# Kernel optimization log

Hardware: AMD Instinct MI355X
Metric: run time of the kernel (lower is better)

Reference implementation:

```python
import jax, jax.numpy as jnp
import numpy as np

P = 1_500_000
N_DEPTH = 6 * 118 * 16 * 44  # 498432 flattened depth bins
N_FEAT = 6 * 16 * 44         # 4224 flattened feature rows
TOTAL_BEV = 40000            # 200x200 BEV grid
C = 80


def setup_inputs() -> dict:
    key = jax.random.key(0)
    k1, k2, k3, k4, k5, k6, k7 = jax.random.split(key, 7)
    depth = jax.random.uniform(k1, (6, 118, 16, 44), dtype=jnp.float32)
    feat = jax.random.normal(k2, (6, 16, 44, C), dtype=jnp.float32)
    ranks_depth = jax.random.randint(k3, (P,), 0, N_DEPTH, dtype=jnp.int64)
    ranks_feat = jax.random.randint(k4, (P,), 0, N_FEAT, dtype=jnp.int64)
    ranks_bev = jnp.sort(jax.random.randint(k5, (P,), 0, TOTAL_BEV, dtype=jnp.int64))
    interval_starts = jnp.sort(jax.random.randint(k6, (TOTAL_BEV,), 0, P, dtype=jnp.int64))
    interval_lengths = jax.random.randint(k7, (TOTAL_BEV,), 0, 64, dtype=jnp.int64)
    return {
        "depth": depth,
        "feat": feat,
        "ranks_depth": ranks_depth,
        "ranks_feat": ranks_feat,
        "ranks_bev": ranks_bev,
        "interval_starts": interval_starts,
        "interval_lengths": interval_lengths,
        "total_bev": TOTAL_BEV,
    }


def reference(depth, feat, ranks_depth, ranks_feat, ranks_bev,
              interval_starts, interval_lengths, total_bev):
    # interval_starts / interval_lengths are unused (as in the torch source)
    channels = feat.shape[-1]
    feat_flat = feat.reshape(-1, channels).astype(jnp.float32)   # [N_feat, C]
    depth_flat = depth.reshape(-1).astype(jnp.float32)           # [N_depth]
    gathered_feat = feat_flat[ranks_feat]                        # [P, C]
    gathered_depth = depth_flat[ranks_depth][:, None]            # [P, 1]
    weighted_feat = gathered_feat * gathered_depth               # [P, C]
    out = jax.ops.segment_sum(weighted_feat, ranks_bev,
                              num_segments=int(total_bev))       # [total_bev, C]
    return out
```

## Files before the change

kernel.cpp:

```cpp
#include <hip/hip_runtime.h>


#define CHN 80
#define SSTRIDE 84

__global__ __launch_bounds__(256)
void seg_starts_kernel(const int* __restrict__ rb, int* __restrict__ seg,
                       int P, int total_bev) {
    int q = blockIdx.x * blockDim.x + threadIdx.x;
    int i4 = q * 4;
    if (i4 >= P) return;
    const int4 v = *reinterpret_cast<const int4*>(rb + i4);
    int prev = (i4 == 0) ? -1 : rb[i4 - 1];
    int cur;
    cur = v.x; for (int b = prev + 1; b <= cur; ++b) seg[b] = i4 + 0; prev = cur;
    cur = v.y; for (int b = prev + 1; b <= cur; ++b) seg[b] = i4 + 1; prev = cur;
    cur = v.z; for (int b = prev + 1; b <= cur; ++b) seg[b] = i4 + 2; prev = cur;
    cur = v.w; for (int b = prev + 1; b <= cur; ++b) seg[b] = i4 + 3; prev = cur;
    if (i4 + 4 >= P) {
        for (int b = prev + 1; b <= total_bev; ++b) seg[b] = P;
    }
}

__global__ __launch_bounds__(256)
void bev_pool_kernel(const float* __restrict__ depth,
                     const float* __restrict__ feat,
                     const int* __restrict__ rd,
                     const int* __restrict__ rf,
                     const int* __restrict__ seg,
                     float* __restrict__ out,
                     int total_bev) {
    __shared__ float lds_buf[4][16 * SSTRIDE];

    const int wave = threadIdx.x >> 6;
    const int lane = threadIdx.x & 63;
    const int bin = blockIdx.x * 4 + wave;
    if (bin >= total_bev) return;

    const int slot = lane >> 2;
    const int ll   = lane & 3;

    const int lo = seg[bin];
    const int hi = seg[bin + 1];

    float4 a0 = make_float4(0.f, 0.f, 0.f, 0.f);
    float4 a1 = a0, a2 = a0, a3 = a0, a4 = a0;

    int i = lo + slot;
    bool valid = i < hi;
    int di = 0, fi = 0;
    if (valid) { di = rd[i]; fi = rf[i]; }
    while (valid) {
        const int ni = i + 16;
        const bool nvalid = ni < hi;
        int ndi = 0, nfi = 0;
        if (nvalid) { ndi = rd[ni]; nfi = rf[ni]; }

        const float d = depth[di];
        const float4* frow = reinterpret_cast<const float4*>(feat + (size_t)fi * CHN) + ll;
        const float4 f0 = frow[0];
        const float4 f1 = frow[4];
        const float4 f2 = frow[8];
        const float4 f3 = frow[12];
        const float4 f4 = frow[16];
        a0.x += d * f0.x; a0.y += d * f0.y; a0.z += d * f0.z; a0.w += d * f0.w;
        a1.x += d * f1.x; a1.y += d * f1.y; a1.z += d * f1.z; a1.w += d * f1.w;
        a2.x += d * f2.x; a2.y += d * f2.y; a2.z += d * f2.z; a2.w += d * f2.w;
        a3.x += d * f3.x; a3.y += d * f3.y; a3.z += d * f3.z; a3.w += d * f3.w;
        a4.x += d * f4.x; a4.y += d * f4.y; a4.z += d * f4.z; a4.w += d * f4.w;

        i = ni; di = ndi; fi = nfi; valid = nvalid;
    }

    {
        float* wb = &lds_buf[wave][slot * SSTRIDE + 4 * ll];
        *reinterpret_cast<float4*>(wb +  0) = a0;
        *reinterpret_cast<float4*>(wb + 16) = a1;
        *reinterpret_cast<float4*>(wb + 32) = a2;
        *reinterpret_cast<float4*>(wb + 48) = a3;
        *reinterpret_cast<float4*>(wb + 64) = a4;
    }
    const int g = lane >> 5;
    const int c = lane & 31;
    float4 r = make_float4(0.f, 0.f, 0.f, 0.f);
    if (c < 20) {
        const float* rp = &lds_buf[wave][g * 8 * SSTRIDE + c * 4];
        #pragma unroll
        for (int t = 0; t < 8; ++t) {
            const float4 v = *reinterpret_cast<const float4*>(rp + t * SSTRIDE);
            r.x += v.x; r.y += v.y; r.z += v.z; r.w += v.w;
        }
    }
    r.x += __shfl_xor(r.x, 32, 64);
    r.y += __shfl_xor(r.y, 32, 64);
    r.z += __shfl_xor(r.z, 32, 64);
    r.w += __shfl_xor(r.w, 32, 64);

    if (lane < 20) {
        *reinterpret_cast<float4*>(out + (size_t)bin * CHN + lane * 4) = r;
    }
}

extern "C" void kernel_launch(void* const* d_in, const int* in_sizes, int n_in,
                              void* d_out, int out_size, void* d_ws, size_t ws_size,
                              hipStream_t stream) {
    const float* depth = (const float*)d_in[0];
    const float* feat  = (const float*)d_in[1];
    const int*   rd    = (const int*)d_in[2];
    const int*   rf    = (const int*)d_in[3];
    const int*   rb    = (const int*)d_in[4];
    float* out = (float*)d_out;

    const int P = in_sizes[2];
    const int total_bev = out_size / CHN;

    int* seg = (int*)d_ws;

    const int quads = (P + 3) / 4;
    seg_starts_kernel<<<(quads + 255) / 256, 256, 0, stream>>>(rb, seg, P, total_bev);
    bev_pool_kernel<<<(total_bev + 3) / 4, 256, 0, stream>>>(depth, feat, rd, rf, seg,
                                                             out, total_bev);
}
```

Measured before the change: 114.6 us.

## Pack features to fp16 rows and pre-gather depth weights before pooling

Adds a pre-pass that converts the feature table to fp16 rows padded to 192 bytes, so the pooling loop reads half the bytes per gathered row. A second pre-pass gathers depth[ranks_depth] into a contiguous array, which turns the dependent random depth load into a streaming read inside the main loop. Which path runs depends on the available workspace size. The costs are two extra kernel launches, an extra P-sized write and read for the weights, and reduced feature precision that could affect accuracy tolerance.

Result: no change. 116.6 us (+1.7%).

```diff
diff --git a/kernel.cpp b/kernel.cpp
--- a/kernel.cpp
+++ b/kernel.cpp
@@ -1,8 +1,47 @@
 #include <hip/hip_runtime.h>
+#include <hip/hip_fp16.h>
 
 
 #define CHN 80
 #define SSTRIDE 84
+#define ROWB 192
+
+struct __align__(8)  h4 { __half2 a, b; };
+struct __align__(16) h8 { __half2 a, b, c, d; };
+
+__global__ __launch_bounds__(256)
+void gather_wd(const float* __restrict__ depth, const int* __restrict__ rd,
+               float* __restrict__ wd, int P) {
+    int q = blockIdx.x * blockDim.x + threadIdx.x;
+    int i4 = q * 4;
+    if (i4 + 3 < P) {
+        const int4 r = *reinterpret_cast<const int4*>(rd + i4);
+        float4 o;
+        o.x = depth[r.x]; o.y = depth[r.y]; o.z = depth[r.z]; o.w = depth[r.w];
+        *reinterpret_cast<float4*>(wd + i4) = o;
+    } else {
+        for (int i = i4; i < P; ++i) wd[i] = depth[rd[i]];
+    }
+}
+
+__global__ __launch_bounds__(256)
+void pack_feat_f16(const float* __restrict__ feat, __half* __restrict__ featp,
+                   int n_chunks ) {
+    int q = blockIdx.x * blockDim.x + threadIdx.x;
+    if (q >= n_chunks) return;
+    const int j = q / 24;
+    const int c = q - j * 24;
+    h4 o;
+    if (c < 20) {
+        const float4 v = *reinterpret_cast<const float4*>(feat + (size_t)j * CHN + c * 4);
+        o.a = __floats2half2_rn(v.x, v.y);
+        o.b = __floats2half2_rn(v.z, v.w);
+    } else {
+        o.a = __floats2half2_rn(0.f, 0.f);
+        o.b = o.a;
+    }
+    *reinterpret_cast<h4*>(reinterpret_cast<char*>(featp) + (size_t)j * ROWB + c * 8) = o;
+}
 
 __global__ __launch_bounds__(256)
 void seg_starts_kernel(const int* __restrict__ rb, int* __restrict__ seg,
@@ -22,9 +61,12 @@
     }
 }
 
+template <int MODE>
 __global__ __launch_bounds__(256)
 void bev_pool_kernel(const float* __restrict__ depth,
                      const float* __restrict__ feat,
+                     const __half* __restrict__ featp,
+                     const float* __restrict__ wd,
                      const int* __restrict__ rd,
                      const int* __restrict__ rf,
                      const int* __restrict__ seg,
@@ -49,36 +91,70 @@
     int i = lo + slot;
     bool valid = i < hi;
     int di = 0, fi = 0;
-    if (valid) { di = rd[i]; fi = rf[i]; }
+    float dv = 0.f;
+    if (valid) {
+        fi = rf[i];
+        if constexpr (MODE == 2) dv = wd[i]; else di = rd[i];
+    }
     while (valid) {
         const int ni = i + 16;
         const bool nvalid = ni < hi;
         int ndi = 0, nfi = 0;
-        if (nvalid) { ndi = rd[ni]; nfi = rf[ni]; }
-
-        const float d = depth[di];
-        const float4* frow = reinterpret_cast<const float4*>(feat + (size_t)fi * CHN) + ll;
-        const float4 f0 = frow[0];
-        const float4 f1 = frow[4];
-        const float4 f2 = frow[8];
-        const float4 f3 = frow[12];
-        const float4 f4 = frow[16];
-        a0.x += d * f0.x; a0.y += d * f0.y; a0.z += d * f0.z; a0.w += d * f0.w;
-        a1.x += d * f1.x; a1.y += d * f1.y; a1.z += d * f1.z; a1.w += d * f1.w;
-        a2.x += d * f2.x; a2.y += d * f2.y; a2.z += d * f2.z; a2.w += d * f2.w;
-        a3.x += d * f3.x; a3.y += d * f3.y; a3.z += d * f3.z; a3.w += d * f3.w;
-        a4.x += d * f4.x; a4.y += d * f4.y; a4.z += d * f4.z; a4.w += d * f4.w;
-
-        i = ni; di = ndi; fi = nfi; valid = nvalid;
+        float ndv = 0.f;
+        if (nvalid) {
+            nfi = rf[ni];
+            if constexpr (MODE == 2) ndv = wd[ni]; else ndi = rd[ni];
+        }
+
+        const float d = (MODE == 2) ? dv : depth[di];
+        if constexpr (MODE >= 1) {
+            const char* rowp = reinterpret_cast<const char*>(featp) + (size_t)fi * ROWB;
+            const h8 u0 = *reinterpret_cast<const h8*>(rowp + (ll << 4));
+            const h8 u1 = *reinterpret_cast<const h8*>(rowp + 64 + (ll << 4));
+            const h4 u2 = *reinterpret_cast<const h4*>(rowp + 128 + (ll << 3));
+            float2 p, q;
+            p = __half22float2(u0.a); q = __half22float2(u0.b);
+            a0.x += d*p.x; a0.y += d*p.y; a0.z += d*q.x; a0.w += d*q.y;
+            p = __half22float2(u0.c); q = __half22float2(u0.d);
+            a1.x += d*p.x; a1.y += d*p.y; a1.z += d*q.x; a1.w += d*q.y;
+            p = __half22float2(u1.a); q = __half22float2(u1.b);
+            a2.x += d*p.x; a2.y += d*p.y; a2.z += d*q.x; a2.w += d*q.y;
+            p = __half22float2(u1.c); q = __half22float2(u1.d);
+            a3.x += d*p.x; a3.y += d*p.y; a3.z += d*q.x; a3.w += d*q.y;
+            p = __half22float2(u2.a); q = __half22float2(u2.b);
+            a4.x += d*p.x; a4.y += d*p.y; a4.z += d*q.x; a4.w += d*q.y;
+        } else {
+            const float4* frow = reinterpret_cast<const float4*>(feat + (size_t)fi * CHN) + ll;
+            const float4 f0 = frow[0];
+            const float4 f1 = frow[4];
+            const float4 f2 = frow[8];
+            const float4 f3 = frow[12];
+            const float4 f4 = frow[16];
+            a0.x += d * f0.x; a0.y += d * f0.y; a0.z += d * f0.z; a0.w += d * f0.w;
+            a1.x += d * f1.x; a1.y += d * f1.y; a1.z += d * f1.z; a1.w += d * f1.w;
+            a2.x += d * f2.x; a2.y += d * f2.y; a2.z += d * f2.z; a2.w += d * f2.w;
+            a3.x += d * f3.x; a3.y += d * f3.y; a3.z += d * f3.z; a3.w += d * f3.w;
+            a4.x += d * f4.x; a4.y += d * f4.y; a4.z += d * f4.z; a4.w += d * f4.w;
+        }
+
+        i = ni; di = ndi; fi = nfi; dv = ndv; valid = nvalid;
     }
 
     {
-        float* wb = &lds_buf[wave][slot * SSTRIDE + 4 * ll];
-        *reinterpret_cast<float4*>(wb +  0) = a0;
-        *reinterpret_cast<float4*>(wb + 16) = a1;
-        *reinterpret_cast<float4*>(wb + 32) = a2;
-        *reinterpret_cast<float4*>(wb + 48) = a3;
-        *reinterpret_cast<float4*>(wb + 64) = a4;
+        float* wb = &lds_buf[wave][slot * SSTRIDE];
+        if constexpr (MODE >= 1) {
+            *reinterpret_cast<float4*>(wb + 8 * ll)      = a0;
+            *reinterpret_cast<float4*>(wb + 8 * ll + 4)  = a1;
+            *reinterpret_cast<float4*>(wb + 32 + 8 * ll) = a2;
+            *reinterpret_cast<float4*>(wb + 36 + 8 * ll) = a3;
+            *reinterpret_cast<float4*>(wb + 64 + 4 * ll) = a4;
+        } else {
+            *reinterpret_cast<float4*>(wb + 4 * ll)      = a0;
+            *reinterpret_cast<float4*>(wb + 4 * ll + 16) = a1;
+            *reinterpret_cast<float4*>(wb + 4 * ll + 32) = a2;
+            *reinterpret_cast<float4*>(wb + 4 * ll + 48) = a3;
+            *reinterpret_cast<float4*>(wb + 4 * ll + 64) = a4;
+        }
     }
     const int g = lane >> 5;
     const int c = lane & 31;
@@ -112,12 +188,37 @@
     float* out = (float*)d_out;
 
     const int P = in_sizes[2];
+    const int feat_elems = in_sizes[1];
+    const int n_rows = feat_elems / CHN;
     const int total_bev = out_size / CHN;
 
     int* seg = (int*)d_ws;
+    const size_t seg_bytes   = ((size_t)(total_bev + 1) * 4 + 255) & ~(size_t)255;
+    const size_t featp_bytes = (((size_t)n_rows * ROWB) + 255) & ~(size_t)255;
+    const size_t need_B = seg_bytes + featp_bytes;
+    const size_t need_A = need_B + (size_t)P * 4;
+    __half* featp = (__half*)((char*)d_ws + seg_bytes);
+    float*  wd    = (float*)((char*)d_ws + seg_bytes + featp_bytes);
+
+    const bool rows_ok = (feat_elems % CHN) == 0;
+    const int mode = (!rows_ok) ? 0 : (ws_size >= need_A) ? 2 : (ws_size >= need_B) ? 1 : 0;
 
     const int quads = (P + 3) / 4;
+    if (mode == 2) {
+        gather_wd<<<(quads + 255) / 256, 256, 0, stream>>>(depth, rd, wd, P);
+    }
+    if (mode >= 1) {
+        const int n_chunks = n_rows * 24;
+        pack_feat_f16<<<(n_chunks + 255) / 256, 256, 0, stream>>>(feat, featp, n_chunks);
+    }
     seg_starts_kernel<<<(quads + 255) / 256, 256, 0, stream>>>(rb, seg, P, total_bev);
-    bev_pool_kernel<<<(total_bev + 3) / 4, 256, 0, stream>>>(depth, feat, rd, rf, seg,
-                                                             out, total_bev);
-}
+
+    const int grid = (total_bev + 3) / 4;
+    if (mode == 2) {
+        bev_pool_kernel<2><<<grid, 256, 0, stream>>>(depth, feat, featp, wd, rd, rf, seg, out, total_bev);
+    } else if (mode == 1) {
+        bev_pool_kernel<1><<<grid, 256, 0, stream>>>(depth, feat, featp, wd, rd, rf, seg, out, total_bev);
+    } else {
+        bev_pool_kernel<0><<<grid, 256, 0, stream>>>(depth, feat, featp, wd, rd, rf, seg, out, total_bev);
+    }
+}
```

## Stage fp16 feature channel slices in LDS and pre-gather depth weights

Applied to the files above, without the earlier changes.

Adds a pre-pass that gathers depth[ranks_depth] into a contiguous workspace array. The main kernel splits the 80 channels into 10 groups of 8, and each block stages all feature rows for its group in LDS as fp16. Each block then processes a chunk of bins, reading features from LDS instead of doing random global float4 gathers. This costs an extra kernel launch and P*4 bytes of workspace, re-reads rf/wd ten times (once per channel group), and reduces feature precision to half.

Result: slower. 289.6 us (+152.7%).

```diff
diff --git a/kernel.cpp b/kernel.cpp
--- a/kernel.cpp
+++ b/kernel.cpp
@@ -1,8 +1,30 @@
 #include <hip/hip_runtime.h>
+#include <hip/hip_fp16.h>
 
 
 #define CHN 80
+#define NROWS_MAX 4224
+#define NGROUPS 10
+#define GCH 8
+#define BINS_PER_BLK 784
 #define SSTRIDE 84
+
+struct __align__(16) h8 { __half2 a, b, c, d; };
+
+__global__ __launch_bounds__(256)
+void gather_wd(const float* __restrict__ depth, const int* __restrict__ rd,
+               float* __restrict__ wd, int P) {
+    int q = blockIdx.x * blockDim.x + threadIdx.x;
+    int i4 = q * 4;
+    if (i4 + 3 < P) {
+        const int4 r = *reinterpret_cast<const int4*>(rd + i4);
+        float4 o;
+        o.x = depth[r.x]; o.y = depth[r.y]; o.z = depth[r.z]; o.w = depth[r.w];
+        *reinterpret_cast<float4*>(wd + i4) = o;
+    } else {
+        for (int i = i4; i < P; ++i) wd[i] = depth[rd[i]];
+    }
+}
 
 __global__ __launch_bounds__(256)
 void seg_starts_kernel(const int* __restrict__ rb, int* __restrict__ seg,
@@ -22,24 +44,90 @@
     }
 }
 
+__global__ __launch_bounds__(512, 4)
+void bev_pool_lds(const float* __restrict__ feat,
+                  const float* __restrict__ wd,
+                  const int* __restrict__ rf,
+                  const int* __restrict__ seg,
+                  float* __restrict__ out,
+                  int total_bev, int n_rows, int nchunks) {
+    __shared__ __half lfeat[NROWS_MAX * GCH];
+
+    const int g     = blockIdx.x / nchunks;
+    const int chunk = blockIdx.x - g * nchunks;
+
+    for (int r = threadIdx.x; r < n_rows; r += 512) {
+        const float* src = feat + (size_t)r * CHN + g * GCH;
+        const float4 u = *reinterpret_cast<const float4*>(src);
+        const float4 v = *reinterpret_cast<const float4*>(src + 4);
+        h8 o;
+        o.a = __floats2half2_rn(u.x, u.y);
+        o.b = __floats2half2_rn(u.z, u.w);
+        o.c = __floats2half2_rn(v.x, v.y);
+        o.d = __floats2half2_rn(v.z, v.w);
+        *reinterpret_cast<h8*>(&lfeat[r * GCH]) = o;
+    }
+    __syncthreads();
+
+    const int wave = threadIdx.x >> 6;
+    const int lane = threadIdx.x & 63;
+    const int slot = lane >> 2;
+    const int ll   = lane & 3;
+
+    const int bin_lo = chunk * BINS_PER_BLK;
+    const int bin_hi = min(bin_lo + BINS_PER_BLK, total_bev);
+
+    for (int bin = bin_lo + wave; bin < bin_hi; bin += 8) {
+        const int lo = seg[bin];
+        const int hi = seg[bin + 1];
+
+        float ax = 0.f, ay = 0.f;
+
+        int i = lo + slot;
+        bool valid = i < hi;
+        int fi = 0; float dv = 0.f;
+        if (valid) { fi = rf[i]; dv = wd[i]; }
+        while (valid) {
+            const int ni = i + 16;
+            const bool nvalid = ni < hi;
+            int nfi = 0; float ndv = 0.f;
+            if (nvalid) { nfi = rf[ni]; ndv = wd[ni]; }
+
+            const __half2 hv = *reinterpret_cast<const __half2*>(&lfeat[fi * GCH + ll * 2]);
+            const float2 f2 = __half22float2(hv);
+            ax += dv * f2.x;
+            ay += dv * f2.y;
+
+            i = ni; fi = nfi; dv = ndv; valid = nvalid;
+        }
+
+        #pragma unroll
+        for (int ofs = 4; ofs <= 32; ofs <<= 1) {
+            ax += __shfl_xor(ax, ofs, 64);
+            ay += __shfl_xor(ay, ofs, 64);
+        }
+        if (lane < 4) {
+            float2 o; o.x = ax; o.y = ay;
+            *reinterpret_cast<float2*>(out + (size_t)bin * CHN + g * GCH + ll * 2) = o;
+        }
+    }
+}
+
 __global__ __launch_bounds__(256)
-void bev_pool_kernel(const float* __restrict__ depth,
-                     const float* __restrict__ feat,
-                     const int* __restrict__ rd,
-                     const int* __restrict__ rf,
-                     const int* __restrict__ seg,
-                     float* __restrict__ out,
-                     int total_bev) {
+void bev_pool_f32(const float* __restrict__ depth,
+                  const float* __restrict__ feat,
+                  const int* __restrict__ rd,
+                  const int* __restrict__ rf,
+                  const int* __restrict__ seg,
+                  float* __restrict__ out,
+                  int total_bev) {
     __shared__ float lds_buf[4][16 * SSTRIDE];
-
     const int wave = threadIdx.x >> 6;
     const int lane = threadIdx.x & 63;
     const int bin = blockIdx.x * 4 + wave;
     if (bin >= total_bev) return;
-
     const int slot = lane >> 2;
     const int ll   = lane & 3;
-
     const int lo = seg[bin];
     const int hi = seg[bin + 1];
 
@@ -55,23 +143,16 @@
         const bool nvalid = ni < hi;
         int ndi = 0, nfi = 0;
         if (nvalid) { ndi = rd[ni]; nfi = rf[ni]; }
-
         const float d = depth[di];
         const float4* frow = reinterpret_cast<const float4*>(feat + (size_t)fi * CHN) + ll;
-        const float4 f0 = frow[0];
-        const float4 f1 = frow[4];
-        const float4 f2 = frow[8];
-        const float4 f3 = frow[12];
-        const float4 f4 = frow[16];
-        a0.x += d * f0.x; a0.y += d * f0.y; a0.z += d * f0.z; a0.w += d * f0.w;
-        a1.x += d * f1.x; a1.y += d * f1.y; a1.z += d * f1.z; a1.w += d * f1.w;
-        a2.x += d * f2.x; a2.y += d * f2.y; a2.z += d * f2.z; a2.w += d * f2.w;
-        a3.x += d * f3.x; a3.y += d * f3.y; a3.z += d * f3.z; a3.w += d * f3.w;
-        a4.x += d * f4.x; a4.y += d * f4.y; a4.z += d * f4.z; a4.w += d * f4.w;
-
+        const float4 f0 = frow[0], f1 = frow[4], f2 = frow[8], f3 = frow[12], f4 = frow[16];
+        a0.x += d*f0.x; a0.y += d*f0.y; a0.z += d*f0.z; a0.w += d*f0.w;
+        a1.x += d*f1.x; a1.y += d*f1.y; a1.z += d*f1.z; a1.w += d*f1.w;
+        a2.x += d*f2.x; a2.y += d*f2.y; a2.z += d*f2.z; a2.w += d*f2.w;
+        a3.x += d*f3.x; a3.y += d*f3.y; a3.z += d*f3.z; a3.w += d*f3.w;
+        a4.x += d*f4.x; a4.y += d*f4.y; a4.z += d*f4.z; a4.w += d*f4.w;
         i = ni; di = ndi; fi = nfi; valid = nvalid;
     }
-
     {
         float* wb = &lds_buf[wave][slot * SSTRIDE + 4 * ll];
         *reinterpret_cast<float4*>(wb +  0) = a0;
@@ -95,7 +176,6 @@
     r.y += __shfl_xor(r.y, 32, 64);
     r.z += __shfl_xor(r.z, 32, 64);
     r.w += __shfl_xor(r.w, 32, 64);
-
     if (lane < 20) {
         *reinterpret_cast<float4*>(out + (size_t)bin * CHN + lane * 4) = r;
     }
@@ -112,12 +192,28 @@
     float* out = (float*)d_out;
 
     const int P = in_sizes[2];
+    const int feat_elems = in_sizes[1];
+    const int n_rows = feat_elems / CHN;
     const int total_bev = out_size / CHN;
 
     int* seg = (int*)d_ws;
+    const size_t seg_bytes = ((size_t)(total_bev + 1) * 4 + 255) & ~(size_t)255;
+    const size_t need = seg_bytes + (size_t)P * 4;
+    float* wd = (float*)((char*)d_ws + seg_bytes);
+
+    const bool lds_ok = (feat_elems % CHN) == 0 && n_rows <= NROWS_MAX &&
+                        ws_size >= need;
 
     const int quads = (P + 3) / 4;
-    seg_starts_kernel<<<(quads + 255) / 256, 256, 0, stream>>>(rb, seg, P, total_bev);
-    bev_pool_kernel<<<(total_bev + 3) / 4, 256, 0, stream>>>(depth, feat, rd, rf, seg,
-                                                             out, total_bev);
-}
+    if (lds_ok) {
+        gather_wd<<<(quads + 255) / 256, 256, 0, stream>>>(depth, rd, wd, P);
+        seg_starts_kernel<<<(quads + 255) / 256, 256, 0, stream>>>(rb, seg, P, total_bev);
+        const int nchunks = (total_bev + BINS_PER_BLK - 1) / BINS_PER_BLK;
+        bev_pool_lds<<<NGROUPS * nchunks, 512, 0, stream>>>(
+            feat, wd, rf, seg, out, total_bev, n_rows, nchunks);
+    } else {
+        seg_starts_kernel<<<(quads + 255) / 256, 256, 0, stream>>>(rb, seg, P, total_bev);
+        bev_pool_f32<<<(total_bev + 3) / 4, 256, 0, stream>>>(
+            depth, feat, rd, rf, seg, out, total_bev);
+    }
+}
```
